# Kernel tuning notes

Measured on AMD Instinct MI355X. Metric: run time of the kernel, lower is better.

Reference implementation:

```python
import jax, jax.numpy as jnp
import numpy as np

H = 512

def _lstm_scan(xs, h0, c0, Wih, Whh, bih, bhh):
    # xs: [T,B,I]; PyTorch gate order i,f,g,o
    def step(carry, x):
        h, c = carry
        gates = x @ Wih.T + bih + h @ Whh.T + bhh  # [B,4H]
        i, f, g, o = jnp.split(gates, 4, axis=-1)
        c = jax.nn.sigmoid(f) * c + jax.nn.sigmoid(i) * jnp.tanh(g)
        h = jax.nn.sigmoid(o) * jnp.tanh(c)
        return (h, c), h
    (h, c), ys = jax.lax.scan(step, (h0, c0), xs)
    return ys, h, c


def setup_inputs() -> dict:
    key = jax.random.key(0)
    ks = jax.random.split(key, 12)
    T, B, I, O = 513, 128, 1, 1
    s = 1.0 / np.sqrt(H)
    u = lambda k, shp: jax.random.uniform(k, shp, jnp.float32, -s, s)
    return {
        "input_seq": jax.random.normal(ks[0], (T, B, I), jnp.float32),
        "h0": jnp.zeros((B, H), jnp.float32),
        "c0": jnp.zeros((B, H), jnp.float32),
        "lstm_Wih": u(ks[1], (4 * H, I)),
        "lstm_Whh": u(ks[2], (4 * H, H)),
        "lstm_bih": u(ks[3], (4 * H,)),
        "lstm_bhh": u(ks[4], (4 * H,)),
        "rnn_Wih": u(ks[5], (H, O)),
        "rnn_Whh": u(ks[6], (H, H)),
        "rnn_bih": u(ks[7], (H,)),
        "rnn_bhh": u(ks[8], (H,)),
        "lin_W": u(ks[9], (O, H)),
        "lin_b": u(ks[10], (O,)),
        "batch_size": 128,
        "pred_length": 32,
    }


def reference(input_seq, h0, c0, lstm_Wih, lstm_Whh, lstm_bih, lstm_bhh,
              rnn_Wih, rnn_Whh, rnn_bih, rnn_bhh, lin_W, lin_b,
              batch_size, pred_length):
    # Encoder LSTM over input_seq[:-1]
    enc_ys, h_enc, _ = _lstm_scan(input_seq[:-1], h0, c0,
                                  lstm_Wih, lstm_Whh, lstm_bih, lstm_bhh)
    enc_bth = jnp.transpose(enc_ys, (1, 0, 2))  # [B,T,H]

    def dec_step(carry, _):
        x, h = carry  # x: [B,1] last prediction, h: [B,H] RNN hidden
        h = jnp.tanh(x @ rnn_Wih.T + rnn_bih + h @ rnn_Whh.T + rnn_bhh)
        # Luong dot-product attention over encoder outputs
        scores = jnp.einsum('bth,bh->bt', enc_bth, h)
        w = jax.nn.softmax(scores, axis=-1)
        ctx = jnp.einsum('bt,bth->bh', w, enc_bth)
        out = jax.nn.relu(ctx @ lin_W.T + lin_b)  # [B,1]
        return (out, h), out

    x0 = input_seq[-1]  # [B,1]
    _, preds = jax.lax.scan(dec_step, (x0, h_enc), None, length=pred_length)
    return preds  # [pred_length, B, 1]
```

## Files before the change

### kernel.cpp

```cpp
#include <hip/hip_runtime.h>
#include <hip/hip_bf16.h>

typedef unsigned short u16;
typedef unsigned int u32;
typedef unsigned long long u64;

#define HD 512
#define BATCH 128
#define TENC 512
#define WPAD 520

typedef float f32x4 __attribute__((ext_vector_type(4)));
typedef short s16x8 __attribute__((ext_vector_type(8)));

__device__ __forceinline__ u16 f2b(float f) {
    u32 u = __float_as_uint(f);
    u32 r = (u + 0x7FFFu + ((u >> 16) & 1u)) >> 16;
    return (u16)r;
}
__device__ __forceinline__ float b2f(u16 h) {
    return __uint_as_float(((u32)h) << 16);
}
__device__ __forceinline__ float sigm(float z) { return 1.0f / (1.0f + __expf(-z)); }
__device__ __forceinline__ float tanh_f(float z) { return 1.0f - 2.0f / (__expf(2.0f * z) + 1.0f); }

__global__ void init_misc(const float* __restrict__ h0, const float* __restrict__ rWhh,
                          u64* __restrict__ hb64, u16* __restrict__ rT) {
    int idx = blockIdx.x * 256 + threadIdx.x;
    if (idx < 65536) {
        int g   = idx >> 13;
        int r   = idx & 8191;
        int p   = r >> 12;
        int ofs = r & 4095;
        int b   = ofs >> 8, jp = ofs & 255;
        u64 v = 0ull;
        if (p == 0) {
            const float* hrow = h0 + (size_t)(g * 16 + b) * HD + jp * 2;
            u32 lo = (u32)f2b(hrow[0]) | ((u32)f2b(hrow[1]) << 16);
            v = (u64)lo;
        }
        hb64[(size_t)(g * 2 + p) * 4096 + b * 256 + jp] = v;
    }
    for (int i = idx; i < 262144; i += 131072) {
        int k = i >> 9, j = i & 511;
        rT[i] = f2b(rWhh[j * 512 + k]);
    }
}

__global__ __launch_bounds__(512, 2) void enc_lstm(
    const float* __restrict__ xseq, const float* __restrict__ c0,
    const float* __restrict__ Wih, const float* __restrict__ Whh,
    const float* __restrict__ bih, const float* __restrict__ bhh,
    u16* __restrict__ enc, u64* __restrict__ hb64) {

    __shared__ u16 hlds[16 * WPAD];
    __shared__ float exg[16 * 132];
    __shared__ float bias_l[128];
    __shared__ float wih_l[128];

    const int tid = threadIdx.x;
    const int g = blockIdx.x & 7;
    const int sl = blockIdx.x >> 3;

    if (tid < 128) {
        int n = (tid >> 5) * 512 + sl * 32 + (tid & 31);
        bias_l[tid] = bih[n] + bhh[n];
        wih_l[tid] = Wih[n];
    }

    const int bT = tid >> 5, jl = tid & 31;
    float c = c0[(g * 16 + bT) * HD + sl * 32 + jl];

    const int lane = tid & 63, wv = tid >> 6;
    const int q = lane >> 4, cl = lane & 15;
    const int R = (wv >> 1) * 32 + (wv & 1) * 16;

    s16x8 bw[16];
    {
        int r = R + cl;
        int grow = (r >> 5) * 512 + sl * 32 + (r & 31);
        const float* wrow = Whh + (size_t)grow * 512;
        #pragma unroll
        for (int ks = 0; ks < 16; ++ks) {
            s16x8 v;
            #pragma unroll
            for (int j = 0; j < 8; ++j)
                v[j] = (short)f2b(wrow[ks * 32 + q * 8 + j]);
            bw[ks] = v;
        }
    }

    u32* hlds32 = (u32*)hlds;
    __syncthreads();

    const int jgl = sl * 32 + jl;
    u64* dpl0 = hb64 + (size_t)(g * 2) * 4096 + bT * 256 + (jgl >> 1);
    u64* dpl1 = dpl0 + 4096;

    for (int t = 0; t < TENC; ++t) {
        const u64* src = hb64 + (size_t)(g * 2 + (t & 1)) * 4096;
        const u32 want = (u32)t;
        u64 vv[8];
        #pragma unroll
        for (int i = 0; i < 8; ++i)
            vv[i] = __hip_atomic_load(src + tid + i * 512, __ATOMIC_RELAXED,
                                      __HIP_MEMORY_SCOPE_AGENT);
        float xv = xseq[t * BATCH + g * 16 + bT];
        for (;;) {
            bool ok = true;
            #pragma unroll
            for (int i = 0; i < 8; ++i) {
                if ((u32)(vv[i] >> 32) != want) {
                    ok = false;
                    vv[i] = __hip_atomic_load(src + tid + i * 512, __ATOMIC_RELAXED,
                                              __HIP_MEMORY_SCOPE_AGENT);
                }
            }
            if (ok) break;
        }
        #pragma unroll
        for (int i = 0; i < 8; ++i) {
            int idx = tid + i * 512;
            hlds32[(idx >> 8) * 260 + (idx & 255)] = (u32)vv[i];
        }
        __syncthreads();

        f32x4 acc0 = {0.f, 0.f, 0.f, 0.f}, acc1 = {0.f, 0.f, 0.f, 0.f};
        #pragma unroll
        for (int ks = 0; ks < 16; ks += 2) {
            s16x8 av0 = *(const s16x8*)&hlds[cl * WPAD + ks * 32 + q * 8];
            s16x8 av1 = *(const s16x8*)&hlds[cl * WPAD + (ks + 1) * 32 + q * 8];
            acc0 = __builtin_amdgcn_mfma_f32_16x16x32_bf16(av0, bw[ks], acc0, 0, 0, 0);
            acc1 = __builtin_amdgcn_mfma_f32_16x16x32_bf16(av1, bw[ks + 1], acc1, 0, 0, 0);
        }
        f32x4 acc = acc0 + acc1;
        #pragma unroll
        for (int r4 = 0; r4 < 4; ++r4)
            exg[(q * 4 + r4) * 132 + R + cl] = acc[r4];
        __syncthreads();

        const float* exb = &exg[bT * 132];
        float gi = exb[jl]      + xv * wih_l[jl]      + bias_l[jl];
        float gf = exb[32 + jl] + xv * wih_l[32 + jl] + bias_l[32 + jl];
        float gg = exb[64 + jl] + xv * wih_l[64 + jl] + bias_l[64 + jl];
        float go = exb[96 + jl] + xv * wih_l[96 + jl] + bias_l[96 + jl];
        c = sigm(gf) * c + sigm(gi) * tanh_f(gg);
        float hv = sigm(go) * tanh_f(c);
        u16 h16 = f2b(hv);

        u32 me = (u32)h16;
        u32 up = (u32)__shfl_down((int)me, 1, 64);
        if ((jl & 1) == 0) {
            u64 word = (u64)(me | (up << 16)) | ((u64)(u32)(t + 1) << 32);
            __hip_atomic_store(((t + 1) & 1) ? dpl1 : dpl0, word,
                               __ATOMIC_RELAXED, __HIP_MEMORY_SCOPE_AGENT);
        }
        enc[((size_t)t * BATCH + g * 16 + bT) * HD + jgl] = h16;
    }
}

__global__ __launch_bounds__(512, 1) void dec_all(
    const float* __restrict__ xlast, const u16* __restrict__ enc,
    const u16* __restrict__ rT, const float* __restrict__ rWih,
    const float* __restrict__ rbih, const float* __restrict__ rbhh,
    const float* __restrict__ linW, const float* __restrict__ linb,
    float* __restrict__ dout) {

    __shared__ float hp[512];
    __shared__ float ctxl[8 * 512];
    __shared__ float red[512];
    __shared__ float mw[8], lw[8];
    __shared__ float xsh;

    const int tid = threadIdx.x;
    const int b = blockIdx.x;
    const int wv = tid >> 6, lane = tid & 63;

    hp[tid] = b2f(enc[(size_t)511 * BATCH * HD + b * HD + tid]);
    float x = xlast[b];
    const float bia = rbih[tid] + rbhh[tid];
    const float wih = rWih[tid];
    const float lwt = linW[tid];
    const float lb = linb[0];
    const uint4* rT4 = (const uint4*)rT;
    const u16* ebase = enc + (size_t)b * HD + lane * 8;
    __syncthreads();

    for (int s = 0; s < 32; ++s) {
        float pa[8] = {0, 0, 0, 0, 0, 0, 0, 0};
        const uint4* base = rT4 + (size_t)(wv * 64) * 64 + lane;
        #pragma unroll 4
        for (int kk = 0; kk < 64; ++kk) {
            float hk = hp[wv * 64 + kk];
            uint4 w = base[kk * 64];
            pa[0] = fmaf(hk, b2f((u16)(w.x & 0xFFFF)), pa[0]);
            pa[1] = fmaf(hk, b2f((u16)(w.x >> 16)),    pa[1]);
            pa[2] = fmaf(hk, b2f((u16)(w.y & 0xFFFF)), pa[2]);
            pa[3] = fmaf(hk, b2f((u16)(w.y >> 16)),    pa[3]);
            pa[4] = fmaf(hk, b2f((u16)(w.z & 0xFFFF)), pa[4]);
            pa[5] = fmaf(hk, b2f((u16)(w.z >> 16)),    pa[5]);
            pa[6] = fmaf(hk, b2f((u16)(w.w & 0xFFFF)), pa[6]);
            pa[7] = fmaf(hk, b2f((u16)(w.w >> 16)),    pa[7]);
        }
        #pragma unroll
        for (int i = 0; i < 8; ++i) ctxl[wv * 512 + lane * 8 + i] = pa[i];
        __syncthreads();

        float a = bia + x * wih;
        #pragma unroll
        for (int i = 0; i < 8; ++i) a += ctxl[i * 512 + tid];
        float hv = tanh_f(a);
        red[tid] = hv;
        __syncthreads();

        float h8[8];
        #pragma unroll
        for (int i = 0; i < 8; ++i) h8[i] = red[lane * 8 + i];
        float m = -1e30f, l = 0.f;
        float acc[8] = {0, 0, 0, 0, 0, 0, 0, 0};

        uint4 buf[8];
        #pragma unroll
        for (int i = 0; i < 8; ++i)
            buf[i] = *(const uint4*)(ebase + (size_t)(i * 8 + wv) * 65536);

        for (int it = 0; it < 8; ++it) {
            uint4 nxt[8];
            if (it < 7) {
                #pragma unroll
                for (int i = 0; i < 8; ++i)
                    nxt[i] = *(const uint4*)(ebase +
                               (size_t)((it + 1) * 64 + i * 8 + wv) * 65536);
            }
            float e[8][8], sp[8];
            #pragma unroll
            for (int i = 0; i < 8; ++i) {
                uint4 ev = buf[i];
                e[i][0] = b2f((u16)(ev.x & 0xFFFF)); e[i][1] = b2f((u16)(ev.x >> 16));
                e[i][2] = b2f((u16)(ev.y & 0xFFFF)); e[i][3] = b2f((u16)(ev.y >> 16));
                e[i][4] = b2f((u16)(ev.z & 0xFFFF)); e[i][5] = b2f((u16)(ev.z >> 16));
                e[i][6] = b2f((u16)(ev.w & 0xFFFF)); e[i][7] = b2f((u16)(ev.w >> 16));
                float sd = 0.f;
                #pragma unroll
                for (int j = 0; j < 8; ++j) sd = fmaf(e[i][j], h8[j], sd);
                sp[i] = sd;
            }
            #pragma unroll
            for (int mk = 1; mk < 64; mk <<= 1) {
                #pragma unroll
                for (int i = 0; i < 8; ++i) sp[i] += __shfl_xor(sp[i], mk, 64);
            }
            float pm = sp[0];
            #pragma unroll
            for (int i = 1; i < 8; ++i) pm = fmaxf(pm, sp[i]);
            if (pm > m) {
                float sc = __expf(m - pm);
                l *= sc;
                #pragma unroll
                for (int j = 0; j < 8; ++j) acc[j] *= sc;
                m = pm;
            }
            #pragma unroll
            for (int i = 0; i < 8; ++i) {
                float p = __expf(sp[i] - m);
                l += p;
                #pragma unroll
                for (int j = 0; j < 8; ++j) acc[j] = fmaf(p, e[i][j], acc[j]);
            }
            if (it < 7) {
                #pragma unroll
                for (int i = 0; i < 8; ++i) buf[i] = nxt[i];
            }
        }
        if (lane == 0) { mw[wv] = m; lw[wv] = l; }
        #pragma unroll
        for (int i = 0; i < 8; ++i) ctxl[wv * HD + lane * 8 + i] = acc[i];
        __syncthreads();

        float M = mw[0];
        #pragma unroll
        for (int i = 1; i < 8; ++i) M = fmaxf(M, mw[i]);
        float L = 0.f, aw[8];
        #pragma unroll
        for (int i = 0; i < 8; ++i) { aw[i] = __expf(mw[i] - M); L += aw[i] * lw[i]; }
        float cj = 0.f;
        #pragma unroll
        for (int i = 0; i < 8; ++i) cj = fmaf(aw[i], ctxl[i * HD + tid], cj);
        float r = cj * lwt;
        #pragma unroll
        for (int mk = 1; mk < 64; mk <<= 1) r += __shfl_xor(r, mk, 64);
        if (lane == 0) red[wv] = r;
        __syncthreads();
        if (tid == 0) {
            float o = (red[0] + red[1] + red[2] + red[3] +
                       red[4] + red[5] + red[6] + red[7]) / L + lb;
            o = fmaxf(o, 0.f);
            dout[s * BATCH + b] = o;
            xsh = o;
        }
        __syncthreads();
        x = xsh;
        hp[tid] = hv;
        __syncthreads();
    }
}

extern "C" void kernel_launch(void* const* d_in, const int* in_sizes, int n_in,
                              void* d_out, int out_size, void* d_ws, size_t ws_size,
                              hipStream_t stream) {
    const float* xseq = (const float*)d_in[0];
    const float* h0   = (const float*)d_in[1];
    const float* c0   = (const float*)d_in[2];
    const float* Wih  = (const float*)d_in[3];
    const float* Whh  = (const float*)d_in[4];
    const float* bih  = (const float*)d_in[5];
    const float* bhh  = (const float*)d_in[6];
    const float* rWih = (const float*)d_in[7];
    const float* rWhh = (const float*)d_in[8];
    const float* rbih = (const float*)d_in[9];
    const float* rbhh = (const float*)d_in[10];
    const float* linW = (const float*)d_in[11];
    const float* linb = (const float*)d_in[12];
    float* dout = (float*)d_out;

    char* ws = (char*)d_ws;
    u16* enc  = (u16*)ws;
    u16* rT   = (u16*)(ws + 67108864);
    u64* hb64 = (u64*)(ws + 67108864 + 524288);

    init_misc<<<512, 256, 0, stream>>>(h0, rWhh, hb64, rT);
    enc_lstm<<<128, 512, 0, stream>>>(xseq, c0, Wih, Whh, bih, bhh, enc, hb64);
    dec_all<<<128, 512, 0, stream>>>(xseq + 512 * BATCH, enc, rT, rWih,
                                     rbih, rbhh, linW, linb, dout);
}
```

Before: 2.372 ms.

## Process four batch groups per encoder block with shared weight registers

The encoder LSTM grid shrinks from 128 to 32 blocks. Each block keeps one 32-column hidden slice of the weights in registers and processes four batch groups in sequence within each timestep. It issues the spin-wait loads for all four groups up front, so their latency overlaps with earlier groups' compute. This cuts the number of participants in the cross-block handoff and reduces weight loading, but each block does four times the serial work per step, which lengthens the critical path.

```diff
diff --git a/kernel.cpp b/kernel.cpp
--- a/kernel.cpp
+++ b/kernel.cpp
@@ -47,7 +47,63 @@
     }
 }
 
-__global__ __launch_bounds__(512, 2) void enc_lstm(
+#define PROC(GI, VV, SRC, XV)                                                 \
+    do {                                                                      \
+        for (;;) {                                                            \
+            bool ok = true;                                                   \
+            _Pragma("unroll")                                                 \
+            for (int i = 0; i < 8; ++i) {                                     \
+                if ((u32)(VV[i] >> 32) != want) {                             \
+                    ok = false;                                               \
+                    VV[i] = __hip_atomic_load(SRC + tid + i * 512,            \
+                                __ATOMIC_RELAXED, __HIP_MEMORY_SCOPE_AGENT);  \
+                }                                                             \
+            }                                                                 \
+            if (ok) break;                                                    \
+        }                                                                     \
+        _Pragma("unroll")                                                     \
+        for (int i = 0; i < 8; ++i) {                                         \
+            int idx = tid + i * 512;                                          \
+            hlds32[(idx >> 8) * 260 + (idx & 255)] = (u32)VV[i];              \
+        }                                                                     \
+        __syncthreads();                                  \
+        f32x4 acc0 = {0.f, 0.f, 0.f, 0.f}, acc1 = {0.f, 0.f, 0.f, 0.f};       \
+        _Pragma("unroll")                                                     \
+        for (int ks = 0; ks < 16; ks += 2) {                                  \
+            s16x8 av0 = *(const s16x8*)&hlds[cl * WPAD + ks * 32 + q * 8];    \
+            s16x8 av1 = *(const s16x8*)&hlds[cl * WPAD + (ks + 1) * 32 + q * 8]; \
+            acc0 = __builtin_amdgcn_mfma_f32_16x16x32_bf16(av0, bw[ks], acc0, 0, 0, 0); \
+            acc1 = __builtin_amdgcn_mfma_f32_16x16x32_bf16(av1, bw[ks + 1], acc1, 0, 0, 0); \
+        }                                                                     \
+        f32x4 accs = acc0 + acc1;                                             \
+        _Pragma("unroll")                                                     \
+        for (int r4 = 0; r4 < 4; ++r4)                                        \
+            exg[(q * 4 + r4) * 132 + R + cl] = accs[r4];                      \
+        __syncthreads();                 \
+        {                                                                     \
+            const float* exb = &exg[bT * 132];                                \
+            float ga = exb[jl]      + XV * wih_l[jl]      + bias_l[jl];       \
+            float gf = exb[32 + jl] + XV * wih_l[32 + jl] + bias_l[32 + jl];  \
+            float gg = exb[64 + jl] + XV * wih_l[64 + jl] + bias_l[64 + jl];  \
+            float go = exb[96 + jl] + XV * wih_l[96 + jl] + bias_l[96 + jl];  \
+            float cc = sigm(gf) * cst[GI] + sigm(ga) * tanh_f(gg);            \
+            cst[GI] = cc;                                                     \
+            float hv = sigm(go) * tanh_f(cc);                                 \
+            u16 h16 = f2b(hv);                                                \
+            u32 me = (u32)h16;                                                \
+            u32 up = (u32)__shfl_down((int)me, 1, 64);                        \
+            if ((jl & 1) == 0) {                                              \
+                u64 word = (u64)(me | (up << 16)) | ((u64)(u32)(t + 1) << 32);\
+                u64* dst = hb64 + (size_t)((p4 + GI) * 2 + ((t + 1) & 1)) * 4096 \
+                                + bT * 256 + (jgl >> 1);                      \
+                __hip_atomic_store(dst, word, __ATOMIC_RELAXED,               \
+                                   __HIP_MEMORY_SCOPE_AGENT);                 \
+            }                                                                 \
+            enc[((size_t)t * BATCH + (p4 + GI) * 16 + bT) * HD + jgl] = h16;  \
+        }                                                                     \
+    } while (0)
+
+__global__ __launch_bounds__(512, 1) void enc_lstm(
     const float* __restrict__ xseq, const float* __restrict__ c0,
     const float* __restrict__ Wih, const float* __restrict__ Whh,
     const float* __restrict__ bih, const float* __restrict__ bhh,
@@ -59,8 +115,8 @@
     __shared__ float wih_l[128];
 
     const int tid = threadIdx.x;
-    const int g = blockIdx.x & 7;
-    const int sl = blockIdx.x >> 3;
+    const int sl = blockIdx.x & 15;
+    const int p4 = (blockIdx.x >> 4) * 4;
 
     if (tid < 128) {
         int n = (tid >> 5) * 512 + sl * 32 + (tid & 31);
@@ -69,7 +125,10 @@
     }
 
     const int bT = tid >> 5, jl = tid & 31;
-    float c = c0[(g * 16 + bT) * HD + sl * 32 + jl];
+    float cst[4];
+    #pragma unroll
+    for (int gi = 0; gi < 4; ++gi)
+        cst[gi] = c0[((p4 + gi) * 16 + bT) * HD + sl * 32 + jl];
 
     const int lane = tid & 63, wv = tid >> 6;
     const int q = lane >> 4, cl = lane & 15;
@@ -94,68 +153,41 @@
     __syncthreads();
 
     const int jgl = sl * 32 + jl;
-    u64* dpl0 = hb64 + (size_t)(g * 2) * 4096 + bT * 256 + (jgl >> 1);
-    u64* dpl1 = dpl0 + 4096;
 
     for (int t = 0; t < TENC; ++t) {
-        const u64* src = hb64 + (size_t)(g * 2 + (t & 1)) * 4096;
         const u32 want = (u32)t;
-        u64 vv[8];
-        #pragma unroll
-        for (int i = 0; i < 8; ++i)
-            vv[i] = __hip_atomic_load(src + tid + i * 512, __ATOMIC_RELAXED,
-                                      __HIP_MEMORY_SCOPE_AGENT);
-        float xv = xseq[t * BATCH + g * 16 + bT];
-        for (;;) {
-            bool ok = true;
-            #pragma unroll
-            for (int i = 0; i < 8; ++i) {
-                if ((u32)(vv[i] >> 32) != want) {
-                    ok = false;
-                    vv[i] = __hip_atomic_load(src + tid + i * 512, __ATOMIC_RELAXED,
-                                              __HIP_MEMORY_SCOPE_AGENT);
-                }
-            }
-            if (ok) break;
-        }
-        #pragma unroll
-        for (int i = 0; i < 8; ++i) {
-            int idx = tid + i * 512;
-            hlds32[(idx >> 8) * 260 + (idx & 255)] = (u32)vv[i];
-        }
-        __syncthreads();
-
-        f32x4 acc0 = {0.f, 0.f, 0.f, 0.f}, acc1 = {0.f, 0.f, 0.f, 0.f};
-        #pragma unroll
-        for (int ks = 0; ks < 16; ks += 2) {
-            s16x8 av0 = *(const s16x8*)&hlds[cl * WPAD + ks * 32 + q * 8];
-            s16x8 av1 = *(const s16x8*)&hlds[cl * WPAD + (ks + 1) * 32 + q * 8];
-            acc0 = __builtin_amdgcn_mfma_f32_16x16x32_bf16(av0, bw[ks], acc0, 0, 0, 0);
-            acc1 = __builtin_amdgcn_mfma_f32_16x16x32_bf16(av1, bw[ks + 1], acc1, 0, 0, 0);
-        }
-        f32x4 acc = acc0 + acc1;
-        #pragma unroll
-        for (int r4 = 0; r4 < 4; ++r4)
-            exg[(q * 4 + r4) * 132 + R + cl] = acc[r4];
-        __syncthreads();
-
-        const float* exb = &exg[bT * 132];
-        float gi = exb[jl]      + xv * wih_l[jl]      + bias_l[jl];
-        float gf = exb[32 + jl] + xv * wih_l[32 + jl] + bias_l[32 + jl];
-        float gg = exb[64 + jl] + xv * wih_l[64 + jl] + bias_l[64 + jl];
-        float go = exb[96 + jl] + xv * wih_l[96 + jl] + bias_l[96 + jl];
-        c = sigm(gf) * c + sigm(gi) * tanh_f(gg);
-        float hv = sigm(go) * tanh_f(c);
-        u16 h16 = f2b(hv);
-
-        u32 me = (u32)h16;
-        u32 up = (u32)__shfl_down((int)me, 1, 64);
-        if ((jl & 1) == 0) {
-            u64 word = (u64)(me | (up << 16)) | ((u64)(u32)(t + 1) << 32);
-            __hip_atomic_store(((t + 1) & 1) ? dpl1 : dpl0, word,
-                               __ATOMIC_RELAXED, __HIP_MEMORY_SCOPE_AGENT);
-        }
-        enc[((size_t)t * BATCH + g * 16 + bT) * HD + jgl] = h16;
+        const u64* s0 = hb64 + (size_t)((p4 + 0) * 2 + (t & 1)) * 4096;
+        const u64* s1 = hb64 + (size_t)((p4 + 1) * 2 + (t & 1)) * 4096;
+        const u64* s2 = hb64 + (size_t)((p4 + 2) * 2 + (t & 1)) * 4096;
+        const u64* s3 = hb64 + (size_t)((p4 + 3) * 2 + (t & 1)) * 4096;
+
+        u64 vv0[8], vv1[8], vv2[8], vv3[8];
+        #pragma unroll
+        for (int i = 0; i < 8; ++i)
+            vv0[i] = __hip_atomic_load(s0 + tid + i * 512, __ATOMIC_RELAXED,
+                                       __HIP_MEMORY_SCOPE_AGENT);
+        #pragma unroll
+        for (int i = 0; i < 8; ++i)
+            vv1[i] = __hip_atomic_load(s1 + tid + i * 512, __ATOMIC_RELAXED,
+                                       __HIP_MEMORY_SCOPE_AGENT);
+        #pragma unroll
+        for (int i = 0; i < 8; ++i)
+            vv2[i] = __hip_atomic_load(s2 + tid + i * 512, __ATOMIC_RELAXED,
+                                       __HIP_MEMORY_SCOPE_AGENT);
+        #pragma unroll
+        for (int i = 0; i < 8; ++i)
+            vv3[i] = __hip_atomic_load(s3 + tid + i * 512, __ATOMIC_RELAXED,
+                                       __HIP_MEMORY_SCOPE_AGENT);
+
+        float xv0 = xseq[t * BATCH + (p4 + 0) * 16 + bT];
+        float xv1 = xseq[t * BATCH + (p4 + 1) * 16 + bT];
+        float xv2 = xseq[t * BATCH + (p4 + 2) * 16 + bT];
+        float xv3 = xseq[t * BATCH + (p4 + 3) * 16 + bT];
+
+        PROC(0, vv0, s0, xv0);
+        PROC(1, vv1, s1, xv1);
+        PROC(2, vv2, s2, xv2);
+        PROC(3, vv3, s3, xv3);
     }
 }
 
@@ -329,7 +361,7 @@
     u64* hb64 = (u64*)(ws + 67108864 + 524288);
 
     init_misc<<<512, 256, 0, stream>>>(h0, rWhh, hb64, rT);
-    enc_lstm<<<128, 512, 0, stream>>>(xseq, c0, Wih, Whh, bih, bhh, enc, hb64);
+    enc_lstm<<<32, 512, 0, stream>>>(xseq, c0, Wih, Whh, bih, bhh, enc, hb64);
     dec_all<<<128, 512, 0, stream>>>(xseq + 512 * BATCH, enc, rT, rWih,
                                      rbih, rbhh, linW, linb, dout);
 }
```

Result: slower. 5.191 ms (+118.9%).
